# Kernel optimization log

Measured on AMD Instinct MI355X. Metric: run time of the kernel, lower is better.

## Reference

```python
import jax, jax.numpy as jnp
import numpy as np

MAX_ITERS = 20
TOL = 1e-3


def best_fit_transform(A, B):
    # A, B: [N, m]; returns homogeneous transform T mapping A -> B.
    m = A.shape[1]
    cA = jnp.mean(A, axis=0)
    cB = jnp.mean(B, axis=0)
    AA = A - cA
    BB = B - cB
    H = AA.T @ BB                      # [m, m] cross-covariance
    U, S, Vt = jnp.linalg.svd(H)
    # reflection fix: if det(R) < 0, flip last row of Vt
    R0 = Vt.T @ U.T
    flip = jnp.linalg.det(R0) < 0
    Vt = Vt.at[m - 1].multiply(jnp.where(flip, -1.0, 1.0).astype(Vt.dtype))
    R = Vt.T @ U.T
    t = cB - R @ cA
    T = jnp.eye(m + 1, dtype=A.dtype).at[:m, :m].set(R).at[:m, m].set(t)
    return T, R, t


def nearest_neighbor(src, dst):
    # src, dst: [N, m]; brute-force 1-NN of each src point in dst.
    d2 = (jnp.sum(src * src, axis=1)[:, None]
          - 2.0 * (src @ dst.T)
          + jnp.sum(dst * dst, axis=1)[None, :])        # [N, N]
    idx = jnp.argmin(d2, axis=1)                          # [N]
    dmin = jnp.take_along_axis(d2, idx[:, None], axis=1)[:, 0]
    dist = jnp.sqrt(jnp.maximum(dmin, 0.0) + 1e-12)
    return dist, idx


def icp(A, B, max_iterations=MAX_ITERS, tolerance=TOL):
    m = A.shape[1]
    N = A.shape[0]
    src0 = jnp.concatenate([A.T, jnp.ones((1, N), A.dtype)], axis=0)  # [m+1, N]

    def step(carry, _):
        src, prev_err, done = carry
        dist, idx = nearest_neighbor(src[:m].T, B)
        T, _, _ = best_fit_transform(src[:m].T, B[idx])
        new_src = T @ src
        err = jnp.mean(dist)
        converged = jnp.abs(prev_err - err) < tolerance
        src = jnp.where(done, src, new_src)
        prev_err = jnp.where(done, prev_err, err)
        done = done | converged
        return (src, prev_err, done), None

    carry0 = (src0, jnp.zeros((), A.dtype), jnp.zeros((), bool))
    (src, _, _), _ = jax.lax.scan(step, carry0, None, length=max_iterations)
    T, _, _ = best_fit_transform(A, src[:m].T)
    return T


def setup_inputs() -> dict:
    key = jax.random.key(0)
    kA, kB = jax.random.split(key)
    A = jax.random.normal(kA, (8192, 3), dtype=jnp.float32)
    B = jax.random.normal(kB, (8192, 3), dtype=jnp.float32)
    return {"A": A, "B": B}


def reference(A, B):
    return icp(A, B)
```

## Files before the change

kernel.cpp:

```cpp
#include <hip/hip_runtime.h>

#define NPTS   8192
#define NB     256
#define NT     256
#define SRCW   8
#define NSTEP  (NPTS / 64)
#define MAXIT  20
#define TOLER  1e-3
#define SPINCAP 200000000u

typedef unsigned long long u64;
typedef unsigned int u32;
typedef float f2 __attribute__((ext_vector_type(2)));

#define WS_PART    0
#define WS_FLAGS   65536

__device__ inline double atom_ld(const double* p) {
  return __hip_atomic_load(p, __ATOMIC_RELAXED, __HIP_MEMORY_SCOPE_AGENT);
}
__device__ inline void atom_st(double* p, double v) {
  __hip_atomic_store(p, v, __ATOMIC_RELAXED, __HIP_MEMORY_SCOPE_AGENT);
}
__device__ inline int atom_ldi(const int* p) {
  return __hip_atomic_load(p, __ATOMIC_RELAXED, __HIP_MEMORY_SCOPE_AGENT);
}
__device__ inline void atom_sti(int* p, int v) {
  __hip_atomic_store(p, v, __ATOMIC_RELAXED, __HIP_MEMORY_SCOPE_AGENT);
}

__device__ void eig3f(const float K[3][3], float w[3], float V[3][3])
{
  const float p1 = K[0][1]*K[0][1] + K[0][2]*K[0][2] + K[1][2]*K[1][2];
  const float q  = (K[0][0] + K[1][1] + K[2][2]) * (1.f/3.f);
  const float p2 = (K[0][0]-q)*(K[0][0]-q) + (K[1][1]-q)*(K[1][1]-q)
                 + (K[2][2]-q)*(K[2][2]-q) + 2.f*p1;
  if (p2 < 1e-20f) {
    w[0]=w[1]=w[2]=q;
    V[0][0]=1;V[1][0]=0;V[2][0]=0; V[0][1]=0;V[1][1]=1;V[2][1]=0;
    V[0][2]=0;V[1][2]=0;V[2][2]=1;
    return;
  }
  const float p = sqrtf(p2 * (1.f/6.f));
  const float ip = 1.f / p;
  float Bm[3][3];
  for (int i = 0; i < 3; ++i)
    for (int j = 0; j < 3; ++j)
      Bm[i][j] = (K[i][j] - ((i==j) ? q : 0.f)) * ip;
  float detB = Bm[0][0]*(Bm[1][1]*Bm[2][2] - Bm[1][2]*Bm[2][1])
             - Bm[0][1]*(Bm[1][0]*Bm[2][2] - Bm[1][2]*Bm[2][0])
             + Bm[0][2]*(Bm[1][0]*Bm[2][1] - Bm[1][1]*Bm[2][0]);
  float r = fminf(1.f, fmaxf(-1.f, detB * 0.5f));
  const float phi = acosf(r) * (1.f/3.f);
  w[0] = q + 2.f*p*cosf(phi);
  w[2] = q + 2.f*p*cosf(phi + 2.0943951023931953f);
  w[1] = 3.f*q - w[0] - w[2];
  for (int kk = 0; kk < 2; ++kk) {
    const int k = (kk == 0) ? 0 : 2;
    float lam = w[k];
    float r0[3] = {K[0][0]-lam, K[0][1], K[0][2]};
    float r1[3] = {K[1][0], K[1][1]-lam, K[1][2]};
    float r2[3] = {K[2][0], K[2][1], K[2][2]-lam};
    float c01[3] = {r0[1]*r1[2]-r0[2]*r1[1], r0[2]*r1[0]-r0[0]*r1[2], r0[0]*r1[1]-r0[1]*r1[0]};
    float c12[3] = {r1[1]*r2[2]-r1[2]*r2[1], r1[2]*r2[0]-r1[0]*r2[2], r1[0]*r2[1]-r1[1]*r2[0]};
    float c20[3] = {r2[1]*r0[2]-r2[2]*r0[1], r2[2]*r0[0]-r2[0]*r0[2], r2[0]*r0[1]-r2[1]*r0[0]};
    float n01 = c01[0]*c01[0]+c01[1]*c01[1]+c01[2]*c01[2];
    float n12 = c12[0]*c12[0]+c12[1]*c12[1]+c12[2]*c12[2];
    float n20 = c20[0]*c20[0]+c20[1]*c20[1]+c20[2]*c20[2];
    float* best = c01; float nb = n01;
    if (n12 > nb) { best = c12; nb = n12; }
    if (n20 > nb) { best = c20; nb = n20; }
    float inv = 1.f / sqrtf(nb + 1e-30f);
    V[0][k]=best[0]*inv; V[1][k]=best[1]*inv; V[2][k]=best[2]*inv;
  }
  V[0][1] = V[1][2]*V[2][0] - V[2][2]*V[1][0];
  V[1][1] = V[2][2]*V[0][0] - V[0][2]*V[2][0];
  V[2][1] = V[0][2]*V[1][0] - V[1][2]*V[0][0];
  float nm = sqrtf(V[0][1]*V[0][1]+V[1][1]*V[1][1]+V[2][1]*V[2][1]) + 1e-30f;
  V[0][1] /= nm; V[1][1] /= nm; V[2][1] /= nm;
}

__device__ void kabsch_Rf(const float H[3][3], float R[3][3])
{
  float K[3][3];
  for (int i = 0; i < 3; ++i)
    for (int j = 0; j < 3; ++j) {
      float s = 0.f;
      for (int k = 0; k < 3; ++k) s += H[k][i] * H[k][j];
      K[i][j] = s;
    }
  float w[3], V[3][3];
  eig3f(K, w, V);
  float U[3][3];
  for (int k = 0; k < 3; ++k) {
    float u0 = H[0][0]*V[0][k] + H[0][1]*V[1][k] + H[0][2]*V[2][k];
    float u1 = H[1][0]*V[0][k] + H[1][1]*V[1][k] + H[1][2]*V[2][k];
    float u2 = H[2][0]*V[0][k] + H[2][1]*V[1][k] + H[2][2]*V[2][k];
    float n = sqrtf(u0*u0 + u1*u1 + u2*u2);
    if (n > 1e-18f) { u0 /= n; u1 /= n; u2 /= n; }
    else if (k == 2) {
      u0 = U[1][0]*U[2][1] - U[2][0]*U[1][1];
      u1 = U[2][0]*U[0][1] - U[0][0]*U[2][1];
      u2 = U[0][0]*U[1][1] - U[1][0]*U[0][1];
      float n2 = sqrtf(u0*u0 + u1*u1 + u2*u2) + 1e-30f;
      u0 /= n2; u1 /= n2; u2 /= n2;
    } else {
      u0 = (k == 0) ? 1.f : 0.f; u1 = (k == 1) ? 1.f : 0.f; u2 = 0.f;
    }
    U[0][k] = u0; U[1][k] = u1; U[2][k] = u2;
  }
  float R0[3][3];
  for (int i = 0; i < 3; ++i)
    for (int j = 0; j < 3; ++j)
      R0[i][j] = V[i][0]*U[j][0] + V[i][1]*U[j][1] + V[i][2]*U[j][2];
  float det = R0[0][0]*(R0[1][1]*R0[2][2] - R0[1][2]*R0[2][1])
            - R0[0][1]*(R0[1][0]*R0[2][2] - R0[1][2]*R0[2][0])
            + R0[0][2]*(R0[1][0]*R0[2][1] - R0[1][1]*R0[2][0]);
  if (det < 0.f)
    for (int i = 0; i < 3; ++i)
      for (int j = 0; j < 3; ++j)
        R0[i][j] -= 2.f * V[i][2] * U[j][2];
  for (int i = 0; i < 3; ++i)
    for (int j = 0; j < 3; ++j)
      R[i][j] = R0[i][j];
}

__device__ inline void flag_barrier(int* flags, int blk, int gen,
                                    int tid, int wav, int lane)
{
  __syncthreads();
  if (tid == 0) {
    __threadfence();
    atom_sti(&flags[blk], gen);
  }
  if (wav == 0) {
    const int base = lane * 4;
    u32 spins = 0;
    bool ok = false;
    while (!ok && spins < SPINCAP) {
      int f0 = atom_ldi(&flags[base + 0]);
      int f1 = atom_ldi(&flags[base + 1]);
      int f2_ = atom_ldi(&flags[base + 2]);
      int f3 = atom_ldi(&flags[base + 3]);
      ok = __all((f0 >= gen) && (f1 >= gen) && (f2_ >= gen) && (f3 >= gen));
      if (!ok) __builtin_amdgcn_s_sleep(2);
      ++spins;
    }
  }
  __syncthreads();
  __threadfence();
}

__global__ __launch_bounds__(NT, 1)
void icp_all(const float* __restrict__ A, const float* __restrict__ B,
             char* __restrict__ ws, float* __restrict__ out)
{
  double* partials = (double*)(ws + WS_PART);
  int*    flags    = (int*)(ws + WS_FLAGS);

  __shared__ __align__(16) float4 bp_lds[NPTS];
  __shared__ double red1[32 * 16];
  __shared__ double red2[4 * 16];
  __shared__ float  Tl[12];
  __shared__ int    dl;

  const int tid  = threadIdx.x;
  const int blk  = blockIdx.x;
  const int wav  = tid >> 6;
  const int lane = tid & 63;
  const int qbase = blk * 32 + wav * SRCW;

  for (int i = tid; i < NPTS; i += NT) {
    float bx = B[3*i], by = B[3*i+1], bz = B[3*i+2];
    bp_lds[i] = make_float4(2.f*bx, 2.f*by, 2.f*bz, bx*bx + by*by + bz*bz);
  }

  float ax[8], ay[8], az[8], sx[8], sy[8], sz[8];
  #pragma unroll
  for (int i = 0; i < 8; ++i) {
    int p = qbase + i;
    ax[i] = A[3*p]; ay[i] = A[3*p+1]; az[i] = A[3*p+2];
    sx[i] = ax[i];  sy[i] = ay[i];    sz[i] = az[i];
  }
  __syncthreads();

  double prev_err = 0.0;
  int it = 0;
  for (; it < MAXIT; ++it) {
    const int par = it & 1;
    f2 nsx2[4], nsy2[4], nsz2[4];
    #pragma unroll
    for (int k = 0; k < 4; ++k) {
      f2 vx = { -sx[2*k], -sx[2*k+1] };
      f2 vy = { -sy[2*k], -sy[2*k+1] };
      f2 vz = { -sz[2*k], -sz[2*k+1] };
      nsx2[k] = vx; nsy2[k] = vy; nsz2[k] = vz;
    }

    float emin[8]; int imin[8];
    #pragma unroll
    for (int i = 0; i < 8; ++i) { emin[i] = 3.4e38f; imin[i] = 0; }

    float4 dcur = bp_lds[lane];
    #pragma unroll 4
    for (int stp = 0; stp < NSTEP - 1; ++stp) {
      float4 dnxt = bp_lds[(stp + 1) * 64 + lane];
      const int jg = stp * 64 + lane;
      f2 dx2 = { dcur.x, dcur.x };
      f2 dy2 = { dcur.y, dcur.y };
      f2 dz2 = { dcur.z, dcur.z };
      f2 dw2 = { dcur.w, dcur.w };
      #pragma unroll
      for (int k = 0; k < 4; ++k) {
        f2 e2 = __builtin_elementwise_fma(nsx2[k], dx2,
                 __builtin_elementwise_fma(nsy2[k], dy2,
                  __builtin_elementwise_fma(nsz2[k], dz2, dw2)));
        float e0 = e2.x, e1 = e2.y;
        if (e0 < emin[2*k])   { emin[2*k]   = e0; imin[2*k]   = jg; }
        if (e1 < emin[2*k+1]) { emin[2*k+1] = e1; imin[2*k+1] = jg; }
      }
      dcur = dnxt;
    }
    {
      const int jg = (NSTEP - 1) * 64 + lane;
      f2 dx2 = { dcur.x, dcur.x };
      f2 dy2 = { dcur.y, dcur.y };
      f2 dz2 = { dcur.z, dcur.z };
      f2 dw2 = { dcur.w, dcur.w };
      #pragma unroll
      for (int k = 0; k < 4; ++k) {
        f2 e2 = __builtin_elementwise_fma(nsx2[k], dx2,
                 __builtin_elementwise_fma(nsy2[k], dy2,
                  __builtin_elementwise_fma(nsz2[k], dz2, dw2)));
        float e0 = e2.x, e1 = e2.y;
        if (e0 < emin[2*k])   { emin[2*k]   = e0; imin[2*k]   = jg; }
        if (e1 < emin[2*k+1]) { emin[2*k+1] = e1; imin[2*k+1] = jg; }
      }
    }
    #pragma unroll
    for (int m = 1; m < 64; m <<= 1) {
      #pragma unroll
      for (int i = 0; i < 8; ++i) {
        float eo = __shfl_xor(emin[i], m, 64);
        int   io = __shfl_xor(imin[i], m, 64);
        if (eo < emin[i] || (eo == emin[i] && io < imin[i])) { emin[i] = eo; imin[i] = io; }
      }
    }

    #pragma unroll
    for (int i = 0; i < 8; ++i) {
      if (lane == i) {
        float s2 = sx[i]*sx[i] + sy[i]*sy[i] + sz[i]*sz[i];
        float d2 = emin[i] + s2;
        float dist = sqrtf(fmaxf(d2, 0.f) + 1e-12f);
        float4 d = bp_lds[imin[i]];
        float bx = 0.5f*d.x, by = 0.5f*d.y, bz = 0.5f*d.z;
        double* r = red1 + (wav * 8 + i) * 16;
        r[0]=sx[i]; r[1]=sy[i]; r[2]=sz[i];
        r[3]=bx;    r[4]=by;    r[5]=bz;
        r[6]=(double)sx[i]*bx;  r[7]=(double)sx[i]*by;  r[8]=(double)sx[i]*bz;
        r[9]=(double)sy[i]*bx;  r[10]=(double)sy[i]*by; r[11]=(double)sy[i]*bz;
        r[12]=(double)sz[i]*bx; r[13]=(double)sz[i]*by; r[14]=(double)sz[i]*bz;
        r[15]=dist;
      }
    }
    __syncthreads();
    if (tid < 16) {
      double ssum = 0.0;
      for (int g = 0; g < 32; ++g) ssum += red1[g * 16 + tid];
      atom_st(&partials[((size_t)par * 16 + tid) * NB + blk], ssum);
    }
    flag_barrier(flags, blk, it + 1, tid, wav, lane);

    {
      double a2[16];
      #pragma unroll
      for (int k = 0; k < 16; ++k)
        a2[k] = atom_ld(&partials[((size_t)par * 16 + k) * NB + tid]);
      for (int m = 1; m < 64; m <<= 1) {
        #pragma unroll
        for (int k = 0; k < 16; ++k) a2[k] += __shfl_xor(a2[k], m, 64);
      }
      if (lane == 0)
        for (int k = 0; k < 16; ++k) red2[wav * 16 + k] = a2[k];
    }
    __syncthreads();
    if (tid == 0) {
      double S[16];
      for (int k = 0; k < 16; ++k)
        S[k] = red2[k] + red2[16+k] + red2[32+k] + red2[48+k];
      const double invN = 1.0 / NPTS;
      double cAv[3] = {S[0]*invN, S[1]*invN, S[2]*invN};
      double cBv[3] = {S[3]*invN, S[4]*invN, S[5]*invN};
      float H[3][3];
      for (int i = 0; i < 3; ++i)
        for (int j = 0; j < 3; ++j)
          H[i][j] = (float)(S[6 + i*3 + j] - (double)NPTS * cAv[i] * cBv[j]);
      double err = S[15] * invN;
      int conv = (fabs(prev_err - err) < TOLER) ? 1 : 0;
      prev_err = err;
      float R[3][3];
      kabsch_Rf(H, R);
      float t0 = (float)cBv[0] - (R[0][0]*(float)cAv[0] + R[0][1]*(float)cAv[1] + R[0][2]*(float)cAv[2]);
      float t1 = (float)cBv[1] - (R[1][0]*(float)cAv[0] + R[1][1]*(float)cAv[1] + R[1][2]*(float)cAv[2]);
      float t2 = (float)cBv[2] - (R[2][0]*(float)cAv[0] + R[2][1]*(float)cAv[1] + R[2][2]*(float)cAv[2]);
      Tl[0]=R[0][0]; Tl[1]=R[0][1]; Tl[2]=R[0][2];
      Tl[3]=R[1][0]; Tl[4]=R[1][1]; Tl[5]=R[1][2];
      Tl[6]=R[2][0]; Tl[7]=R[2][1]; Tl[8]=R[2][2];
      Tl[9]=t0; Tl[10]=t1; Tl[11]=t2;
      dl = conv;
    }
    __syncthreads();
    {
      float r00=Tl[0],r01=Tl[1],r02=Tl[2],r10=Tl[3],r11=Tl[4],r12=Tl[5];
      float r20=Tl[6],r21=Tl[7],r22=Tl[8],t0=Tl[9],t1=Tl[10],t2=Tl[11];
      int done = dl;
      #pragma unroll
      for (int i = 0; i < 8; ++i) {
        float nx = r00*sx[i] + r01*sy[i] + r02*sz[i] + t0;
        float ny = r10*sx[i] + r11*sy[i] + r12*sz[i] + t1;
        float nz = r20*sx[i] + r21*sy[i] + r22*sz[i] + t2;
        sx[i]=nx; sy[i]=ny; sz[i]=nz;
      }
      if (done) break;
    }
  }

  const int fpar = (it < MAXIT) ? ((it + 1) & 1) : (MAXIT & 1);
  const int fgen = (it < MAXIT) ? (it + 2) : (MAXIT + 1);
  __syncthreads();
  #pragma unroll
  for (int i = 0; i < 8; ++i) {
    if (lane == i) {
      double* r = red1 + (wav * 8 + i) * 16;
      r[0]=ax[i]; r[1]=ay[i]; r[2]=az[i];
      r[3]=sx[i]; r[4]=sy[i]; r[5]=sz[i];
      r[6]=(double)ax[i]*sx[i];  r[7]=(double)ax[i]*sy[i];  r[8]=(double)ax[i]*sz[i];
      r[9]=(double)ay[i]*sx[i];  r[10]=(double)ay[i]*sy[i]; r[11]=(double)ay[i]*sz[i];
      r[12]=(double)az[i]*sx[i]; r[13]=(double)az[i]*sy[i]; r[14]=(double)az[i]*sz[i];
      r[15]=0.0;
    }
  }
  __syncthreads();
  if (tid < 16) {
    double ssum = 0.0;
    for (int g = 0; g < 32; ++g) ssum += red1[g * 16 + tid];
    atom_st(&partials[((size_t)fpar * 16 + tid) * NB + blk], ssum);
  }
  if (blk != 0) {
    __syncthreads();
    if (tid == 0) { __threadfence(); atom_sti(&flags[blk], fgen); }
    return;
  }
  flag_barrier(flags, blk, fgen, tid, wav, lane);

  double a2[16];
  #pragma unroll
  for (int k = 0; k < 16; ++k)
    a2[k] = atom_ld(&partials[((size_t)fpar * 16 + k) * NB + tid]);
  for (int m = 1; m < 64; m <<= 1) {
    #pragma unroll
    for (int k = 0; k < 16; ++k) a2[k] += __shfl_xor(a2[k], m, 64);
  }
  if (lane == 0)
    for (int k = 0; k < 16; ++k) red2[wav * 16 + k] = a2[k];
  __syncthreads();
  if (tid == 0) {
    double S[16];
    for (int k = 0; k < 16; ++k)
      S[k] = red2[k] + red2[16+k] + red2[32+k] + red2[48+k];
    const double invN = 1.0 / NPTS;
    double cAv[3] = {S[0]*invN, S[1]*invN, S[2]*invN};
    double cSv[3] = {S[3]*invN, S[4]*invN, S[5]*invN};
    float H[3][3];
    for (int i = 0; i < 3; ++i)
      for (int j = 0; j < 3; ++j)
        H[i][j] = (float)(S[6 + i*3 + j] - (double)NPTS * cAv[i] * cSv[j]);
    float R[3][3];
    kabsch_Rf(H, R);
    float u0 = (float)cSv[0] - (R[0][0]*(float)cAv[0] + R[0][1]*(float)cAv[1] + R[0][2]*(float)cAv[2]);
    float u1 = (float)cSv[1] - (R[1][0]*(float)cAv[0] + R[1][1]*(float)cAv[1] + R[1][2]*(float)cAv[2]);
    float u2 = (float)cSv[2] - (R[2][0]*(float)cAv[0] + R[2][1]*(float)cAv[1] + R[2][2]*(float)cAv[2]);
    out[0]=R[0][0]; out[1]=R[0][1]; out[2]=R[0][2]; out[3]=u0;
    out[4]=R[1][0]; out[5]=R[1][1]; out[6]=R[1][2]; out[7]=u1;
    out[8]=R[2][0]; out[9]=R[2][1]; out[10]=R[2][2]; out[11]=u2;
    out[12]=0.f; out[13]=0.f; out[14]=0.f; out[15]=1.f;
  }
}

extern "C" void kernel_launch(void* const* d_in, const int* in_sizes, int n_in,
                              void* d_out, int out_size, void* d_ws, size_t ws_size,
                              hipStream_t stream) {
  const float* A = (const float*)d_in[0];
  const float* B = (const float*)d_in[1];
  float* out = (float*)d_out;
  char* ws = (char*)d_ws;

  hipLaunchKernelGGL(icp_all, dim3(NB), dim3(NT), 0, stream, A, B, ws, out);
}
```

Before: 165.6 us.

## Track per-group minima in NN scan, recover index afterward, parallelize block reductions

The inner nearest-neighbor loop no longer tracks an index per candidate. It keeps a packed-min over 8-candidate groups and records only the winning group index. After the wave reduction it rescans the 8 candidates of the winning group to recover the exact index. The per-source covariance terms are now computed by 8 lanes each and written as vectorized double2 stores, and the block reduction uses wave shuffles instead of a 32-step serial loop by 16 threads. This cuts compare/select work in the hot loop and serial reduction latency. The cost is a recomputation step, and tie-breaking among equal distances may differ from the original lowest-index rule.

```diff
diff --git a/kernel.cpp b/kernel.cpp
--- a/kernel.cpp
+++ b/kernel.cpp
@@ -4,7 +4,7 @@
 #define NB     256
 #define NT     256
 #define SRCW   8
-#define NSTEP  (NPTS / 64)
+#define NG8    16
 #define MAXIT  20
 #define TOLER  1e-3
 #define SPINCAP 200000000u
@@ -12,6 +12,7 @@
 typedef unsigned long long u64;
 typedef unsigned int u32;
 typedef float f2 __attribute__((ext_vector_type(2)));
+typedef double dbl2 __attribute__((ext_vector_type(2)));
 
 #define WS_PART    0
 #define WS_FLAGS   65536
@@ -159,7 +160,7 @@
   int*    flags    = (int*)(ws + WS_FLAGS);
 
   __shared__ __align__(16) float4 bp_lds[NPTS];
-  __shared__ double red1[32 * 16];
+  __shared__ __align__(16) double red1[32 * 16];
   __shared__ double red2[4 * 16];
   __shared__ float  Tl[12];
   __shared__ int    dl;
@@ -197,77 +198,131 @@
       nsx2[k] = vx; nsy2[k] = vy; nsz2[k] = vz;
     }
 
-    float emin[8]; int imin[8];
-    #pragma unroll
-    for (int i = 0; i < 8; ++i) { emin[i] = 3.4e38f; imin[i] = 0; }
-
-    float4 dcur = bp_lds[lane];
-    #pragma unroll 4
-    for (int stp = 0; stp < NSTEP - 1; ++stp) {
-      float4 dnxt = bp_lds[(stp + 1) * 64 + lane];
-      const int jg = stp * 64 + lane;
-      f2 dx2 = { dcur.x, dcur.x };
-      f2 dy2 = { dcur.y, dcur.y };
-      f2 dz2 = { dcur.z, dcur.z };
-      f2 dw2 = { dcur.w, dcur.w };
+    float emin[8]; int gmin[8];
+    #pragma unroll
+    for (int i = 0; i < 8; ++i) { emin[i] = 3.4e38f; gmin[i] = 0; }
+
+    float4 dd[8];
+    #pragma unroll
+    for (int m = 0; m < 8; ++m) dd[m] = bp_lds[m * 64 + lane];
+
+    for (int g = 0; g < NG8 - 1; ++g) {
+      f2 run[4];
+      #pragma unroll
+      for (int m = 0; m < 8; ++m) {
+        f2 dx2 = { dd[m].x, dd[m].x };
+        f2 dy2 = { dd[m].y, dd[m].y };
+        f2 dz2 = { dd[m].z, dd[m].z };
+        f2 dw2 = { dd[m].w, dd[m].w };
+        #pragma unroll
+        for (int k = 0; k < 4; ++k) {
+          f2 e2 = __builtin_elementwise_fma(nsx2[k], dx2,
+                   __builtin_elementwise_fma(nsy2[k], dy2,
+                    __builtin_elementwise_fma(nsz2[k], dz2, dw2)));
+          run[k] = (m == 0) ? e2 : __builtin_elementwise_min(run[k], e2);
+        }
+        dd[m] = bp_lds[(g + 1) * 512 + m * 64 + lane];
+      }
       #pragma unroll
       for (int k = 0; k < 4; ++k) {
-        f2 e2 = __builtin_elementwise_fma(nsx2[k], dx2,
-                 __builtin_elementwise_fma(nsy2[k], dy2,
-                  __builtin_elementwise_fma(nsz2[k], dz2, dw2)));
-        float e0 = e2.x, e1 = e2.y;
-        if (e0 < emin[2*k])   { emin[2*k]   = e0; imin[2*k]   = jg; }
-        if (e1 < emin[2*k+1]) { emin[2*k+1] = e1; imin[2*k+1] = jg; }
-      }
-      dcur = dnxt;
+        if (run[k].x < emin[2*k])   gmin[2*k]   = g;
+        emin[2*k]   = fminf(emin[2*k],   run[k].x);
+        if (run[k].y < emin[2*k+1]) gmin[2*k+1] = g;
+        emin[2*k+1] = fminf(emin[2*k+1], run[k].y);
+      }
     }
     {
-      const int jg = (NSTEP - 1) * 64 + lane;
-      f2 dx2 = { dcur.x, dcur.x };
-      f2 dy2 = { dcur.y, dcur.y };
-      f2 dz2 = { dcur.z, dcur.z };
-      f2 dw2 = { dcur.w, dcur.w };
+      const int g = NG8 - 1;
+      f2 run[4];
+      #pragma unroll
+      for (int m = 0; m < 8; ++m) {
+        f2 dx2 = { dd[m].x, dd[m].x };
+        f2 dy2 = { dd[m].y, dd[m].y };
+        f2 dz2 = { dd[m].z, dd[m].z };
+        f2 dw2 = { dd[m].w, dd[m].w };
+        #pragma unroll
+        for (int k = 0; k < 4; ++k) {
+          f2 e2 = __builtin_elementwise_fma(nsx2[k], dx2,
+                   __builtin_elementwise_fma(nsy2[k], dy2,
+                    __builtin_elementwise_fma(nsz2[k], dz2, dw2)));
+          run[k] = (m == 0) ? e2 : __builtin_elementwise_min(run[k], e2);
+        }
+      }
       #pragma unroll
       for (int k = 0; k < 4; ++k) {
-        f2 e2 = __builtin_elementwise_fma(nsx2[k], dx2,
-                 __builtin_elementwise_fma(nsy2[k], dy2,
-                  __builtin_elementwise_fma(nsz2[k], dz2, dw2)));
-        float e0 = e2.x, e1 = e2.y;
-        if (e0 < emin[2*k])   { emin[2*k]   = e0; imin[2*k]   = jg; }
-        if (e1 < emin[2*k+1]) { emin[2*k+1] = e1; imin[2*k+1] = jg; }
-      }
-    }
+        if (run[k].x < emin[2*k])   gmin[2*k]   = g;
+        emin[2*k]   = fminf(emin[2*k],   run[k].x);
+        if (run[k].y < emin[2*k+1]) gmin[2*k+1] = g;
+        emin[2*k+1] = fminf(emin[2*k+1], run[k].y);
+      }
+    }
+
+    int meta[8];
+    #pragma unroll
+    for (int i = 0; i < 8; ++i) meta[i] = (gmin[i] << 6) | lane;
     #pragma unroll
     for (int m = 1; m < 64; m <<= 1) {
       #pragma unroll
       for (int i = 0; i < 8; ++i) {
         float eo = __shfl_xor(emin[i], m, 64);
-        int   io = __shfl_xor(imin[i], m, 64);
-        if (eo < emin[i] || (eo == emin[i] && io < imin[i])) { emin[i] = eo; imin[i] = io; }
-      }
-    }
-
-    #pragma unroll
-    for (int i = 0; i < 8; ++i) {
-      if (lane == i) {
-        float s2 = sx[i]*sx[i] + sy[i]*sy[i] + sz[i]*sz[i];
-        float d2 = emin[i] + s2;
-        float dist = sqrtf(fmaxf(d2, 0.f) + 1e-12f);
-        float4 d = bp_lds[imin[i]];
-        float bx = 0.5f*d.x, by = 0.5f*d.y, bz = 0.5f*d.z;
-        double* r = red1 + (wav * 8 + i) * 16;
-        r[0]=sx[i]; r[1]=sy[i]; r[2]=sz[i];
-        r[3]=bx;    r[4]=by;    r[5]=bz;
-        r[6]=(double)sx[i]*bx;  r[7]=(double)sx[i]*by;  r[8]=(double)sx[i]*bz;
-        r[9]=(double)sy[i]*bx;  r[10]=(double)sy[i]*by; r[11]=(double)sy[i]*bz;
-        r[12]=(double)sz[i]*bx; r[13]=(double)sz[i]*by; r[14]=(double)sz[i]*bz;
-        r[15]=dist;
-      }
+        int   mo = __shfl_xor(meta[i], m, 64);
+        if (eo < emin[i] || (eo == emin[i] && mo < meta[i])) { emin[i] = eo; meta[i] = mo; }
+      }
+    }
+
+    {
+      const int isrc = lane >> 3;
+      float em = emin[0]; int mt = meta[0];
+      float sxi = sx[0], syi = sy[0], szi = sz[0];
+      #pragma unroll
+      for (int k = 1; k < 8; ++k) {
+        const bool p = (isrc == k);
+        em  = p ? emin[k] : em;   mt  = p ? meta[k] : mt;
+        sxi = p ? sx[k]  : sxi;   syi = p ? sy[k]  : syi;   szi = p ? sz[k] : szi;
+      }
+      const int gg = mt >> 6, ll = mt & 63;
+      const int j0 = gg * 512 + ll;
+      int jj = j0;
+      #pragma unroll
+      for (int m = 7; m >= 0; --m) {
+        float4 c = bp_lds[j0 + m * 64];
+        float e = fmaf(-sxi, c.x, fmaf(-syi, c.y, fmaf(-szi, c.z, c.w)));
+        jj = (e == em) ? (j0 + m * 64) : jj;
+      }
+      float4 dmt = bp_lds[jj];
+      const float bxm = 0.5f*dmt.x, bym = 0.5f*dmt.y, bzm = 0.5f*dmt.z;
+      const double dsx = (double)sxi, dsy = (double)syi, dsz = (double)szi;
+      const double dbx = (double)bxm, dby = (double)bym, dbz = (double)bzm;
+      double w0, w1;
+      switch (lane & 7) {
+        case 0: w0 = dsx;       w1 = dsy;       break;
+        case 1: w0 = dsz;       w1 = dbx;       break;
+        case 2: w0 = dby;       w1 = dbz;       break;
+        case 3: w0 = dsx * dbx; w1 = dsx * dby; break;
+        case 4: w0 = dsx * dbz; w1 = dsy * dbx; break;
+        case 5: w0 = dsy * dby; w1 = dsy * dbz; break;
+        case 6: w0 = dsz * dbx; w1 = dsz * dby; break;
+        default: {
+          const float s2 = sxi*sxi + syi*syi + szi*szi;
+          const float d2f = em + s2;
+          w0 = dsz * dbz;
+          w1 = (double)sqrtf(fmaxf(d2f, 0.f) + 1e-12f);
+        } break;
+      }
+      dbl2 wv = { w0, w1 };
+      *(dbl2*)&red1[(wav * 8 + isrc) * 16 + (lane & 7) * 2] = wv;
+    }
+
+    {
+      const int k16 = lane & 15, h = lane >> 4;
+      double s = red1[(wav*8 + h)*16 + k16] + red1[(wav*8 + 4 + h)*16 + k16];
+      s += __shfl_xor(s, 16, 64);
+      s += __shfl_xor(s, 32, 64);
+      if (lane < 16) red2[wav * 16 + k16] = s;
     }
     __syncthreads();
     if (tid < 16) {
-      double ssum = 0.0;
-      for (int g = 0; g < 32; ++g) ssum += red1[g * 16 + tid];
+      double ssum = red2[tid] + red2[16 + tid] + red2[32 + tid] + red2[48 + tid];
       atom_st(&partials[((size_t)par * 16 + tid) * NB + blk], ssum);
     }
     flag_barrier(flags, blk, it + 1, tid, wav, lane);
@@ -328,23 +383,42 @@
 
   const int fpar = (it < MAXIT) ? ((it + 1) & 1) : (MAXIT & 1);
   const int fgen = (it < MAXIT) ? (it + 2) : (MAXIT + 1);
-  __syncthreads();
-  #pragma unroll
-  for (int i = 0; i < 8; ++i) {
-    if (lane == i) {
-      double* r = red1 + (wav * 8 + i) * 16;
-      r[0]=ax[i]; r[1]=ay[i]; r[2]=az[i];
-      r[3]=sx[i]; r[4]=sy[i]; r[5]=sz[i];
-      r[6]=(double)ax[i]*sx[i];  r[7]=(double)ax[i]*sy[i];  r[8]=(double)ax[i]*sz[i];
-      r[9]=(double)ay[i]*sx[i];  r[10]=(double)ay[i]*sy[i]; r[11]=(double)ay[i]*sz[i];
-      r[12]=(double)az[i]*sx[i]; r[13]=(double)az[i]*sy[i]; r[14]=(double)az[i]*sz[i];
-      r[15]=0.0;
-    }
+  {
+    const int isrc = lane >> 3;
+    float axi = ax[0], ayi = ay[0], azi = az[0];
+    float sxi = sx[0], syi = sy[0], szi = sz[0];
+    #pragma unroll
+    for (int k = 1; k < 8; ++k) {
+      const bool p = (isrc == k);
+      axi = p ? ax[k] : axi;  ayi = p ? ay[k] : ayi;  azi = p ? az[k] : azi;
+      sxi = p ? sx[k] : sxi;  syi = p ? sy[k] : syi;  szi = p ? sz[k] : szi;
+    }
+    const double dax = (double)axi, day = (double)ayi, daz = (double)azi;
+    const double dsx = (double)sxi, dsy = (double)syi, dsz = (double)szi;
+    double w0, w1;
+    switch (lane & 7) {
+      case 0: w0 = dax;       w1 = day;       break;
+      case 1: w0 = daz;       w1 = dsx;       break;
+      case 2: w0 = dsy;       w1 = dsz;       break;
+      case 3: w0 = dax * dsx; w1 = dax * dsy; break;
+      case 4: w0 = dax * dsz; w1 = day * dsx; break;
+      case 5: w0 = day * dsy; w1 = day * dsz; break;
+      case 6: w0 = daz * dsx; w1 = daz * dsy; break;
+      default: w0 = daz * dsz; w1 = 0.0;      break;
+    }
+    dbl2 wv = { w0, w1 };
+    *(dbl2*)&red1[(wav * 8 + isrc) * 16 + (lane & 7) * 2] = wv;
+  }
+  {
+    const int k16 = lane & 15, h = lane >> 4;
+    double s = red1[(wav*8 + h)*16 + k16] + red1[(wav*8 + 4 + h)*16 + k16];
+    s += __shfl_xor(s, 16, 64);
+    s += __shfl_xor(s, 32, 64);
+    if (lane < 16) red2[wav * 16 + k16] = s;
   }
   __syncthreads();
   if (tid < 16) {
-    double ssum = 0.0;
-    for (int g = 0; g < 32; ++g) ssum += red1[g * 16 + tid];
+    double ssum = red2[tid] + red2[16 + tid] + red2[32 + tid] + red2[48 + tid];
     atom_st(&partials[((size_t)fpar * 16 + tid) * NB + blk], ssum);
   }
   if (blk != 0) {
```

Result: faster. 142.2 us (-14.1%).
